# Performance work log

Measured on AMD Instinct MI355X. Metric: run time of the kernel, lower is better.

## Reference

```python
import jax, jax.numpy as jnp
import numpy as np

WS = 7       # window size
HEADS = 3
DIM = 96
HEAD_DIM = DIM // HEADS
SCALE = HEAD_DIM ** -0.5


def _rel_pos_index(ws: int) -> np.ndarray:
    # Swin relative position index, flattened to (ws*ws*ws*ws,)
    coords = np.stack(np.meshgrid(np.arange(ws), np.arange(ws), indexing='ij'))  # (2,ws,ws)
    cf = coords.reshape(2, -1)                      # (2, n)
    rel = cf[:, :, None] - cf[:, None, :]           # (2, n, n)
    rel = rel.transpose(1, 2, 0).astype(np.int64)   # (n, n, 2)
    rel[:, :, 0] += ws - 1
    rel[:, :, 1] += ws - 1
    rel[:, :, 0] *= 2 * ws - 1
    return rel.sum(-1).reshape(-1)

_REL_IDX = _rel_pos_index(WS)


def setup_inputs() -> dict:
    key = jax.random.key(0)
    ks = jax.random.split(key, 6)
    return {
        'x': jax.random.normal(ks[0], (64, 56, 56, DIM), jnp.float32),
        'w_qkv': jax.random.normal(ks[1], (DIM, 3 * DIM), jnp.float32) * 0.02,
        'b_qkv': jax.random.normal(ks[2], (3 * DIM,), jnp.float32) * 0.02,
        'rel_pos': jax.random.normal(ks[3], (HEADS, (2 * WS - 1) ** 2), jnp.float32) * 0.02,
        'w_out': jax.random.normal(ks[4], (DIM, DIM), jnp.float32) * 0.02,
        'b_out': jax.random.normal(ks[5], (DIM,), jnp.float32) * 0.02,
    }


def reference(x, w_qkv, b_qkv, rel_pos, w_out, b_out):
    b, H, W, c = x.shape
    h, w = H // WS, W // WS
    n = WS * WS
    # split_into_windows: 'b (p h) (q w) c -> b h w (p q) c' (p outer -> strided windows)
    xw = x.reshape(b, WS, h, WS, w, c).transpose(0, 2, 4, 1, 3, 5).reshape(b, h, w, n, c)
    qkv = xw @ w_qkv + b_qkv                        # (b,h,w,n,3*dim)
    q, k, v = jnp.split(qkv, 3, axis=-1)

    def to_heads(t):  # (b,h,w,n,g*d) -> (b,g,h,w,n,d)
        return t.reshape(b, h, w, n, HEADS, HEAD_DIM).transpose(0, 4, 1, 2, 3, 5)

    q, k, v = to_heads(q) * SCALE, to_heads(k), to_heads(v)
    sim = jnp.einsum('bghwnd,bghwmd->bghwnm', q, k)  # (b,g,h,w,n,n)
    bias = rel_pos[:, _REL_IDX].reshape(HEADS, n, n)  # (g,n,n)
    sim = sim + bias[None, :, None, None]
    att = jax.nn.softmax(sim, axis=-1)
    out = jnp.einsum('bghwnm,bghwmd->bghwnd', att, v)
    out = out.transpose(0, 2, 3, 4, 1, 5).reshape(b, h, w, n, c)
    # merge_windows: inverse of split
    out = out.reshape(b, h, w, WS, WS, c).transpose(0, 3, 1, 4, 2, 5).reshape(b, H, W, c)
    return out @ w_out + b_out
```

## Files before the change

### kernel.cpp

```cpp
#include <hip/hip_runtime.h>
#include <math.h>

#define SCALE 0.17677669529663687f

typedef float f32x4 __attribute__((ext_vector_type(4)));
typedef short s16x8 __attribute__((ext_vector_type(8)));

__device__ __forceinline__ unsigned short f2bf(float f) {
    unsigned int u = __float_as_uint(f);
    u += 0x7fffu + ((u >> 16) & 1u);
    return (unsigned short)(u >> 16);
}
__device__ __forceinline__ unsigned int pk2(float a, float b) {
    return (unsigned int)f2bf(a) | ((unsigned int)f2bf(b) << 16);
}

__global__ void k_prep(const float* __restrict__ wq, const float* __restrict__ wo,
                       const float* __restrict__ rel_pos,
                       unsigned short* __restrict__ wqT, unsigned short* __restrict__ woT,
                       float* __restrict__ bias_exp) {
    int i = blockIdx.x * 256 + threadIdx.x;
    if (i < 27648) {
        int c = i / 96, k = i - c * 96;
        float w = wq[k * 288 + c];
        if (c < 96) w *= SCALE;
        wqT[i] = f2bf(w);
    } else if (i < 36864) {
        int t = i - 27648;
        int c = t / 96, k = t - c * 96;
        woT[t] = f2bf(wo[k * 96 + c]);
    } else if (i < 36864 + 3 * 49 * 64) {
        int t = i - 36864;
        int g = t / 3136, r = t - g * 3136;
        int q = r >> 6, kt = r & 63;
        float v = 0.f;
        if (kt < 49) {
            int qp = q / 7, qq = q - qp * 7;
            int kp = kt / 7, kq = kt - kp * 7;
            v = rel_pos[g * 169 + (qp - kp + 6) * 13 + (qq - kq + 6)];
        }
        bias_exp[t] = v;
    }
}

#define XSTR 104
#define USTR  72

__global__ __launch_bounds__(192, 3) void k_fused(
        const float* __restrict__ x,
        const unsigned short* __restrict__ wqT,
        const float* __restrict__ b_qkv,
        const float* __restrict__ bias_exp,
        const unsigned short* __restrict__ woT,
        const float* __restrict__ b_out,
        float* __restrict__ out) {
    __shared__ unsigned short s_xv[6912];
    __shared__ unsigned short s_u[3][49 * USTR];

    const int tid  = threadIdx.x;
    const int g    = tid >> 6;
    const int lane = tid & 63;
    const int ln   = lane & 15;
    const int kg   = lane >> 4;

    const int win = blockIdx.x;
    const int ww = win & 7, hh = (win >> 3) & 7, b = win >> 6;
    const size_t base = (size_t)b * 3136;

    for (int i = tid; i < 1176; i += 192) {
        const int tok = i / 24, c = i - tok * 24;
        const int p = tok / 7, q = tok - p * 7;
        const float4 v = *(const float4*)(x + (base + (p * 8 + hh) * 56 + q * 8 + ww) * 96 + c * 4);
        uint2 u; u.x = pk2(v.x, v.y); u.y = pk2(v.z, v.w);
        *(uint2*)(s_xv + tok * XSTR + c * 4) = u;
    }
    __syncthreads();

    s16x8 xf[4][3];
#pragma unroll
    for (int t = 0; t < 4; ++t) {
        int tok = 16 * t + ln; if (tok > 48) tok = 48;
#pragma unroll
        for (int ks = 0; ks < 3; ++ks)
            xf[t][ks] = *(const s16x8*)(s_xv + tok * XSTR + 32 * ks + 8 * kg);
    }
    __syncthreads();

    unsigned short* const U  = s_u[g];
    unsigned short* const Vt = s_xv + g * (32 * USTR);

#pragma unroll
    for (int part = 0; part < 2; ++part) {
#pragma unroll
        for (int tc = 0; tc < 2; ++tc) {
            const int col = part * 96 + g * 32 + 16 * tc + ln;
            s16x8 wf[3];
#pragma unroll
            for (int ks = 0; ks < 3; ++ks)
                wf[ks] = *(const s16x8*)(wqT + (size_t)col * 96 + 32 * ks + 8 * kg);
            const float4 bs = *(const float4*)(b_qkv + part * 96 + g * 32 + 16 * tc + 4 * kg);
            const float bm = part ? 1.0f : SCALE;
#pragma unroll
            for (int tt = 0; tt < 4; ++tt) {
                f32x4 a = {bs.x * bm, bs.y * bm, bs.z * bm, bs.w * bm};
#pragma unroll
                for (int ks = 0; ks < 3; ++ks)
                    a = __builtin_amdgcn_mfma_f32_16x16x32_bf16(wf[ks], xf[tt][ks], a, 0, 0, 0);
                if (tt < 3 || ln == 0) {
                    uint2 u; u.x = pk2(a[0], a[1]); u.y = pk2(a[2], a[3]);
                    *(uint2*)(U + (16 * tt + ln) * USTR + part * 40 + 16 * tc + 4 * kg) = u;
                }
            }
        }
    }
#pragma unroll
    for (int tc = 0; tc < 2; ++tc) {
        const int col = 192 + g * 32 + 16 * tc + ln;
        s16x8 wf[3];
#pragma unroll
        for (int ks = 0; ks < 3; ++ks)
            wf[ks] = *(const s16x8*)(wqT + (size_t)col * 96 + 32 * ks + 8 * kg);
        const float bv = b_qkv[col];
#pragma unroll
        for (int tt = 0; tt < 4; ++tt) {
            f32x4 a = {bv, bv, bv, bv};
#pragma unroll
            for (int ks = 0; ks < 3; ++ks)
                a = __builtin_amdgcn_mfma_f32_16x16x32_bf16(xf[tt][ks], wf[ks], a, 0, 0, 0);
            uint2 u; u.x = pk2(a[0], a[1]); u.y = pk2(a[2], a[3]);
            *(uint2*)(Vt + (16 * tc + ln) * USTR + 16 * tt + 4 * kg) = u;
        }
    }

    s16x8 qf[4], kf[4];
#pragma unroll
    for (int t = 0; t < 4; ++t) {
        int tok = 16 * t + ln; if (tok > 48) tok = 48;
        qf[t] = *(const s16x8*)(U + tok * USTR + 8 * kg);
        kf[t] = *(const s16x8*)(U + tok * USTR + 40 + 8 * kg);
    }
    const int qrow[4] = { ln, 16 + ln, 32 + ln, 48 };
    f32x4 sacc[4][4];
#pragma unroll
    for (int tq = 0; tq < 4; ++tq) {
        const float* brow = bias_exp + (g * 49 + qrow[tq]) * 64;
#pragma unroll
        for (int tk = 0; tk < 4; ++tk) {
            const float4 bb = *(const float4*)(brow + 16 * tk + 4 * kg);
            f32x4 c = {bb.x, bb.y, bb.z, bb.w};
            sacc[tk][tq] = __builtin_amdgcn_mfma_f32_16x16x32_bf16(kf[tk], qf[tq], c, 0, 0, 0);
        }
    }
#pragma unroll
    for (int tq = 0; tq < 4; ++tq) {
        sacc[3][tq][1] = -3e38f; sacc[3][tq][2] = -3e38f; sacc[3][tq][3] = -3e38f;
        if (kg) sacc[3][tq][0] = -3e38f;
    }
#pragma unroll
    for (int tq = 0; tq < 4; ++tq) {
        float m0 = fmaxf(fmaxf(sacc[0][tq][0], sacc[0][tq][1]), fmaxf(sacc[0][tq][2], sacc[0][tq][3]));
        float m1 = fmaxf(fmaxf(sacc[1][tq][0], sacc[1][tq][1]), fmaxf(sacc[1][tq][2], sacc[1][tq][3]));
        float m2 = fmaxf(fmaxf(sacc[2][tq][0], sacc[2][tq][1]), fmaxf(sacc[2][tq][2], sacc[2][tq][3]));
        float m3 = fmaxf(fmaxf(sacc[3][tq][0], sacc[3][tq][1]), fmaxf(sacc[3][tq][2], sacc[3][tq][3]));
        float m = fmaxf(fmaxf(m0, m1), fmaxf(m2, m3));
        m = fmaxf(m, __shfl_xor(m, 16));
        m = fmaxf(m, __shfl_xor(m, 32));
        float s = 0.f;
#pragma unroll
        for (int tk = 0; tk < 4; ++tk)
#pragma unroll
            for (int r = 0; r < 4; ++r) {
                const float e = __expf(sacc[tk][tq][r] - m);
                sacc[tk][tq][r] = e; s += e;
            }
        s += __shfl_xor(s, 16);
        s += __shfl_xor(s, 32);
        const float inv = 1.0f / s;
        if (tq < 3 || ln == 0) {
#pragma unroll
            for (int tk = 0; tk < 4; ++tk) {
                uint2 u;
                u.x = pk2(sacc[tk][tq][0] * inv, sacc[tk][tq][1] * inv);
                u.y = pk2(sacc[tk][tq][2] * inv, sacc[tk][tq][3] * inv);
                *(uint2*)(U + (16 * tq + ln) * USTR + 16 * tk + 4 * kg) = u;
            }
        }
    }

    s16x8 pf[4][2], vf[2][2];
#pragma unroll
    for (int tq = 0; tq < 4; ++tq) {
        int pr = 16 * tq + ln; if (pr > 48) pr = 48;
#pragma unroll
        for (int ks = 0; ks < 2; ++ks)
            pf[tq][ks] = *(const s16x8*)(U + pr * USTR + 32 * ks + 8 * kg);
    }
#pragma unroll
    for (int td = 0; td < 2; ++td)
#pragma unroll
        for (int ks = 0; ks < 2; ++ks)
            vf[td][ks] = *(const s16x8*)(Vt + (16 * td + ln) * USTR + 32 * ks + 8 * kg);
#pragma unroll
    for (int td = 0; td < 2; ++td)
#pragma unroll
        for (int tq = 0; tq < 4; ++tq) {
            f32x4 a = {0.f, 0.f, 0.f, 0.f};
            a = __builtin_amdgcn_mfma_f32_16x16x32_bf16(vf[td][0], pf[tq][0], a, 0, 0, 0);
            a = __builtin_amdgcn_mfma_f32_16x16x32_bf16(vf[td][1], pf[tq][1], a, 0, 0, 0);
            const int q = 16 * tq + ln;
            if (q < 49) {
                uint2 u; u.x = pk2(a[0], a[1]); u.y = pk2(a[2], a[3]);
                *(uint2*)(U + q * USTR + 16 * td + 4 * kg) = u;
            }
        }
    __syncthreads();

    s16x8 af[4][3];
#pragma unroll
    for (int tt = 0; tt < 4; ++tt) {
        int tok = 16 * tt + ln; if (tok > 48) tok = 48;
#pragma unroll
        for (int ks = 0; ks < 3; ++ks)
            af[tt][ks] = *(const s16x8*)(s_u[ks] + tok * USTR + 8 * kg);
    }
#pragma unroll
    for (int j = 0; j < 2; ++j) {
        const int tc = 2 * g + j;
        s16x8 wf[3];
#pragma unroll
        for (int ks = 0; ks < 3; ++ks)
            wf[ks] = *(const s16x8*)(woT + (size_t)(16 * tc + ln) * 96 + 32 * ks + 8 * kg);
        const float4 bs = *(const float4*)(b_out + 16 * tc + 4 * kg);
#pragma unroll
        for (int tt = 0; tt < 4; ++tt) {
            f32x4 a = {bs.x, bs.y, bs.z, bs.w};
#pragma unroll
            for (int ks = 0; ks < 3; ++ks)
                a = __builtin_amdgcn_mfma_f32_16x16x32_bf16(wf[ks], af[tt][ks], a, 0, 0, 0);
            const int tok = 16 * tt + ln;
            if (tok < 49) {
                const int p = (tok * 37) >> 8;
                const int q = tok - p * 7;
                float4 o; o.x = a[0]; o.y = a[1]; o.z = a[2]; o.w = a[3];
                *(float4*)(out + (base + (p * 8 + hh) * 56 + q * 8 + ww) * 96 + 16 * tc + 4 * kg) = o;
            }
        }
    }
}

__global__ void winattn_fp32(const float* __restrict__ x,
                             const float* __restrict__ w_qkv,
                             const float* __restrict__ b_qkv,
                             const float* __restrict__ rel_pos,
                             const float* __restrict__ w_out,
                             const float* __restrict__ b_out,
                             float* __restrict__ out) {
    __shared__ float s_x[49][96];
    __shared__ float s_qkv[49][288];
    __shared__ float s_rel[3 * 169];
    const int t = threadIdx.x;
    const int blk = blockIdx.x;
    const int ww = blk & 7, hh = (blk >> 3) & 7, b = blk >> 6;
    for (int i = t; i < 3 * 169; i += 256) s_rel[i] = rel_pos[i];
    const float* xb = x + (size_t)b * 56 * 56 * 96;
    for (int i = t; i < 49 * 24; i += 256) {
        int tok = i / 24, ch4 = i % 24, p = tok / 7, q = tok % 7;
        float4 v = *(const float4*)(xb + (((p * 8 + hh) * 56) + (q * 8 + ww)) * 96 + ch4 * 4);
        *(float4*)(&s_x[tok][ch4 * 4]) = v;
    }
    __syncthreads();
    for (int u = t; u < 504; u += 256) {
        int cg = u % 72, rg = u / 72, col = cg * 4, r0 = rg * 7;
        float4 bq = *(const float4*)(b_qkv + col);
        float acc[7][4];
#pragma unroll
        for (int r = 0; r < 7; ++r) { acc[r][0]=bq.x; acc[r][1]=bq.y; acc[r][2]=bq.z; acc[r][3]=bq.w; }
        for (int k = 0; k < 96; k += 4) {
            float4 w0 = *(const float4*)(w_qkv + (size_t)(k+0)*288 + col);
            float4 w1 = *(const float4*)(w_qkv + (size_t)(k+1)*288 + col);
            float4 w2 = *(const float4*)(w_qkv + (size_t)(k+2)*288 + col);
            float4 w3 = *(const float4*)(w_qkv + (size_t)(k+3)*288 + col);
#pragma unroll
            for (int r = 0; r < 7; ++r) {
                float4 xv = *(const float4*)(&s_x[r0+r][k]);
                acc[r][0] += xv.x*w0.x + xv.y*w1.x + xv.z*w2.x + xv.w*w3.x;
                acc[r][1] += xv.x*w0.y + xv.y*w1.y + xv.z*w2.y + xv.w*w3.y;
                acc[r][2] += xv.x*w0.z + xv.y*w1.z + xv.z*w2.z + xv.w*w3.z;
                acc[r][3] += xv.x*w0.w + xv.y*w1.w + xv.z*w2.w + xv.w*w3.w;
            }
        }
#pragma unroll
        for (int r = 0; r < 7; ++r)
            *(float4*)(&s_qkv[r0+r][col]) = make_float4(acc[r][0],acc[r][1],acc[r][2],acc[r][3]);
    }
    __syncthreads();
    if (t < 147) {
        const int g = t / 49, qi = t - g * 49, pi = qi / 7, qq = qi - pi * 7;
        float qreg[32];
#pragma unroll
        for (int d = 0; d < 32; d += 4) {
            float4 v = *(const float4*)(&s_qkv[qi][g*32 + d]);
            qreg[d]=v.x*SCALE; qreg[d+1]=v.y*SCALE; qreg[d+2]=v.z*SCALE; qreg[d+3]=v.w*SCALE;
        }
        float sim[49]; float m = -1e30f;
        for (int j = 0; j < 49; ++j) {
            float a = 0.f;
            const float* kr = &s_qkv[j][96 + g*32];
#pragma unroll
            for (int d = 0; d < 32; d += 4) {
                float4 kv = *(const float4*)(kr + d);
                a += qreg[d]*kv.x + qreg[d+1]*kv.y + qreg[d+2]*kv.z + qreg[d+3]*kv.w;
            }
            int pj = j / 7, qj = j % 7;
            a += s_rel[g*169 + (pi-pj+6)*13 + (qq-qj+6)];
            sim[j] = a; m = fmaxf(m, a);
        }
        float s = 0.f;
        for (int j = 0; j < 49; ++j) { float e = __expf(sim[j]-m); sim[j]=e; s+=e; }
        float inv = 1.f/s;
        float o[32];
#pragma unroll
        for (int d = 0; d < 32; ++d) o[d] = 0.f;
        for (int j = 0; j < 49; ++j) {
            float p = sim[j];
            const float* vr = &s_qkv[j][192 + g*32];
#pragma unroll
            for (int d = 0; d < 32; d += 4) {
                float4 vv = *(const float4*)(vr + d);
                o[d] += p*vv.x; o[d+1] += p*vv.y; o[d+2] += p*vv.z; o[d+3] += p*vv.w;
            }
        }
#pragma unroll
        for (int d = 0; d < 32; d += 4)
            *(float4*)(&s_x[qi][g*32 + d]) = make_float4(o[d]*inv, o[d+1]*inv, o[d+2]*inv, o[d+3]*inv);
    }
    __syncthreads();
    for (int u = t; u < 336; u += 256) {
        int cg = u % 48, rg = u / 48, col = cg * 2, r0 = rg * 7;
        float b0 = b_out[col], b1 = b_out[col+1];
        float acc[7][2];
#pragma unroll
        for (int r = 0; r < 7; ++r) { acc[r][0]=b0; acc[r][1]=b1; }
        for (int k = 0; k < 96; k += 4) {
            float2 w0 = *(const float2*)(w_out + (size_t)(k+0)*96 + col);
            float2 w1 = *(const float2*)(w_out + (size_t)(k+1)*96 + col);
            float2 w2 = *(const float2*)(w_out + (size_t)(k+2)*96 + col);
            float2 w3 = *(const float2*)(w_out + (size_t)(k+3)*96 + col);
#pragma unroll
            for (int r = 0; r < 7; ++r) {
                float4 xv = *(const float4*)(&s_x[r0+r][k]);
                acc[r][0] += xv.x*w0.x + xv.y*w1.x + xv.z*w2.x + xv.w*w3.x;
                acc[r][1] += xv.x*w0.y + xv.y*w1.y + xv.z*w2.y + xv.w*w3.y;
            }
        }
#pragma unroll
        for (int r = 0; r < 7; ++r)
            *(float2*)(out + (size_t)(((b*56 + rg*8 + hh)*56) + r*8 + ww)*96 + col) =
                make_float2(acc[r][0], acc[r][1]);
    }
}

extern "C" void kernel_launch(void* const* d_in, const int* in_sizes, int n_in,
                              void* d_out, int out_size, void* d_ws, size_t ws_size,
                              hipStream_t stream) {
    const float* x       = (const float*)d_in[0];
    const float* w_qkv   = (const float*)d_in[1];
    const float* b_qkv   = (const float*)d_in[2];
    const float* rel_pos = (const float*)d_in[3];
    const float* w_out   = (const float*)d_in[4];
    const float* b_out   = (const float*)d_in[5];
    float* out = (float*)d_out;

    const size_t WQT_BYTES  = (size_t)288 * 96 * 2;
    const size_t WOT_BYTES  = (size_t)96 * 96 * 2;
    const size_t BIAS_BYTES = (size_t)3 * 49 * 64 * 4;

    if (ws_size >= WQT_BYTES + WOT_BYTES + BIAS_BYTES) {
        unsigned short* wqT = (unsigned short*)d_ws;
        unsigned short* woT = (unsigned short*)((char*)d_ws + WQT_BYTES);
        float* bias_exp     = (float*)((char*)d_ws + WQT_BYTES + WOT_BYTES);
        hipLaunchKernelGGL(k_prep,  dim3(181),  dim3(256), 0, stream,
                           w_qkv, w_out, rel_pos, wqT, woT, bias_exp);
        hipLaunchKernelGGL(k_fused, dim3(4096), dim3(192), 0, stream,
                           x, wqT, b_qkv, bias_exp, woT, b_out, out);
    } else {
        hipLaunchKernelGGL(winattn_fp32, dim3(4096), dim3(256), 0, stream,
                           x, w_qkv, b_qkv, rel_pos, w_out, b_out, out);
    }
}
```

Baseline: 200.3 us.

## Load x fragments directly from global memory, skipping LDS staging

Each wave now reads its input window from global memory straight into MFMA register fragments, converting to bf16 in place, instead of the block cooperatively staging x in shared memory. This removes the LDS round trip and two block barriers, and V gets its own shared buffer. The cost is that every wave loads the full window, tripling global/cache reads, and uncoalesced 32-byte row reads. Wave priority is also raised during the compute phase.

Result: no change. 203.9 us (+1.8%).

```diff
diff --git a/kernel.cpp b/kernel.cpp
--- a/kernel.cpp
+++ b/kernel.cpp
@@ -43,8 +43,8 @@
     }
 }
 
-#define XSTR 104
 #define USTR  72
+#define VSTR  72
 
 __global__ __launch_bounds__(192, 3) void k_fused(
         const float* __restrict__ x,
@@ -54,8 +54,8 @@
         const unsigned short* __restrict__ woT,
         const float* __restrict__ b_out,
         float* __restrict__ out) {
-    __shared__ unsigned short s_xv[6912];
     __shared__ unsigned short s_u[3][49 * USTR];
+    __shared__ unsigned short s_vt[3][32 * VSTR];
 
     const int tid  = threadIdx.x;
     const int g    = tid >> 6;
@@ -67,27 +67,28 @@
     const int ww = win & 7, hh = (win >> 3) & 7, b = win >> 6;
     const size_t base = (size_t)b * 3136;
 
-    for (int i = tid; i < 1176; i += 192) {
-        const int tok = i / 24, c = i - tok * 24;
-        const int p = tok / 7, q = tok - p * 7;
-        const float4 v = *(const float4*)(x + (base + (p * 8 + hh) * 56 + q * 8 + ww) * 96 + c * 4);
-        uint2 u; u.x = pk2(v.x, v.y); u.y = pk2(v.z, v.w);
-        *(uint2*)(s_xv + tok * XSTR + c * 4) = u;
-    }
-    __syncthreads();
+    unsigned short* const U  = s_u[g];
+    unsigned short* const Vt = s_vt[g];
 
     s16x8 xf[4][3];
 #pragma unroll
     for (int t = 0; t < 4; ++t) {
         int tok = 16 * t + ln; if (tok > 48) tok = 48;
-#pragma unroll
-        for (int ks = 0; ks < 3; ++ks)
-            xf[t][ks] = *(const s16x8*)(s_xv + tok * XSTR + 32 * ks + 8 * kg);
-    }
-    __syncthreads();
-
-    unsigned short* const U  = s_u[g];
-    unsigned short* const Vt = s_xv + g * (32 * USTR);
+        const int p = (tok * 37) >> 8;
+        const int q = tok - p * 7;
+        const float* xr = x + (base + (p * 8 + hh) * 56 + q * 8 + ww) * 96;
+#pragma unroll
+        for (int ks = 0; ks < 3; ++ks) {
+            const float4 lo = *(const float4*)(xr + 32 * ks + 8 * kg);
+            const float4 hi = *(const float4*)(xr + 32 * ks + 8 * kg + 4);
+            uint4 u;
+            u.x = pk2(lo.x, lo.y); u.y = pk2(lo.z, lo.w);
+            u.z = pk2(hi.x, hi.y); u.w = pk2(hi.z, hi.w);
+            xf[t][ks] = *(s16x8*)&u;
+        }
+    }
+
+    __builtin_amdgcn_s_setprio(1);
 
 #pragma unroll
     for (int part = 0; part < 2; ++part) {
@@ -128,7 +129,7 @@
             for (int ks = 0; ks < 3; ++ks)
                 a = __builtin_amdgcn_mfma_f32_16x16x32_bf16(xf[tt][ks], wf[ks], a, 0, 0, 0);
             uint2 u; u.x = pk2(a[0], a[1]); u.y = pk2(a[2], a[3]);
-            *(uint2*)(Vt + (16 * tc + ln) * USTR + 16 * tt + 4 * kg) = u;
+            *(uint2*)(Vt + (16 * tc + ln) * VSTR + 16 * tt + 4 * kg) = u;
         }
     }
 
@@ -199,7 +200,7 @@
     for (int td = 0; td < 2; ++td)
 #pragma unroll
         for (int ks = 0; ks < 2; ++ks)
-            vf[td][ks] = *(const s16x8*)(Vt + (16 * td + ln) * USTR + 32 * ks + 8 * kg);
+            vf[td][ks] = *(const s16x8*)(Vt + (16 * td + ln) * VSTR + 32 * ks + 8 * kg);
 #pragma unroll
     for (int td = 0; td < 2; ++td)
 #pragma unroll
@@ -213,6 +214,7 @@
                 *(uint2*)(U + q * USTR + 16 * td + 4 * kg) = u;
             }
         }
+    __builtin_amdgcn_s_setprio(0);
     __syncthreads();
 
     s16x8 af[4][3];
```
